# Performance work log

Measured on AMD Instinct MI355X. Metric: run time of the kernel, lower is better.

The kernel has to match this reference:

```python
import jax, jax.numpy as jnp
import numpy as np

N_ATOMS = 2_000_000
D_IN = 128
N_HIDDEN = 16
N_STRUCT = 20_000


def setup_inputs() -> dict:
    key = jax.random.key(0)
    kx, ks, k0, k1, k2 = jax.random.split(key, 5)
    x = jax.random.normal(kx, (N_ATOMS, D_IN), dtype=jnp.float32)
    structure = jnp.sort(jax.random.randint(ks, (N_ATOMS,), 0, N_STRUCT, dtype=jnp.int32))
    # MLP(nin=128, nout=1, nhidden=16, nlayers=2, bias=False, activation=None):
    # Linear(128->16) -> Linear(16->16) -> Linear(16->1), purely linear stack.
    W0 = jax.random.normal(k0, (D_IN, N_HIDDEN), dtype=jnp.float32) / np.sqrt(D_IN)
    W1 = jax.random.normal(k1, (N_HIDDEN, N_HIDDEN), dtype=jnp.float32) / np.sqrt(N_HIDDEN)
    W2 = jax.random.normal(k2, (N_HIDDEN, 1), dtype=jnp.float32) / np.sqrt(N_HIDDEN)
    return {"x": x, "W0": W0, "W1": W1, "W2": W2,
            "structure": structure, "num_structures": N_STRUCT}


def reference(x, W0, W1, W2, structure, num_structures):
    # per-atom tiny MLP: [N, D] -> [N, 1] -> [N]
    h = x @ W0            # [N, 16]
    h = h @ W1            # [N, 16]
    pred = (h @ W2)[:, 0]  # [N]
    # scatter-sum per structure id (torch index_add_ equivalent)
    per_struct = jax.ops.segment_sum(pred, structure, num_segments=num_structures)
    return per_struct[:, None]  # [n_struct, 1]
```

## Files before the change

kernel.cpp:

```cpp
#include <hip/hip_runtime.h>

#define D_IN 128
#define NH   16

__global__ void prep_kernel(const float* __restrict__ W0,
                            const float* __restrict__ W1,
                            const float* __restrict__ W2,
                            float* __restrict__ w,
                            float* __restrict__ out, int m) {
    int i = blockIdx.x * blockDim.x + threadIdx.x;
    if (i < m) out[i] = 0.f;

    if (blockIdx.x == 0) {
        __shared__ float v1[NH];
        int t = threadIdx.x;
        if (t < NH) {
            float s = 0.f;
            #pragma unroll
            for (int k = 0; k < NH; ++k) s += W1[t * NH + k] * W2[k];
            v1[t] = s;
        }
        __syncthreads();
        if (t < D_IN) {
            float s = 0.f;
            #pragma unroll
            for (int j = 0; j < NH; ++j) s += W0[t * NH + j] * v1[j];
            w[t] = s;
        }
    }
}

__global__ __launch_bounds__(256) void predict_scatter_kernel(
        const float* __restrict__ x,
        const int*   __restrict__ sid,
        const float* __restrict__ w,
        float*       __restrict__ out,
        int n, int nTiles) {
    __shared__ float preds[256];

    const int lane  = threadIdx.x & 63;
    const int hlane = threadIdx.x & 31;
    const int hw    = threadIdx.x >> 5;

    const float4 wv = reinterpret_cast<const float4*>(w)[hlane];

    for (int tile = blockIdx.x; tile < nTiles; tile += gridDim.x) {
        const long long tileBase = (long long)tile * 256;

        if (tileBase + 256 <= (long long)n) {
            #pragma unroll 4
            for (int step = 0; step < 32; ++step) {
                const long long atom = tileBase + hw * 32 + step;
                float4 xv = reinterpret_cast<const float4*>(x)[atom * 32 + hlane];
                float d = xv.x * wv.x + xv.y * wv.y + xv.z * wv.z + xv.w * wv.w;
                #pragma unroll
                for (int off = 16; off >= 1; off >>= 1)
                    d += __shfl_xor(d, off, 32);
                if (hlane == 0) preds[hw * 32 + step] = d;
            }
        } else {
            for (int step = 0; step < 32; ++step) {
                const long long atom = tileBase + hw * 32 + step;
                if (atom < (long long)n) {
                    float4 xv = reinterpret_cast<const float4*>(x)[atom * 32 + hlane];
                    float d = xv.x * wv.x + xv.y * wv.y + xv.z * wv.z + xv.w * wv.w;
                    #pragma unroll
                    for (int off = 16; off >= 1; off >>= 1)
                        d += __shfl_xor(d, off, 32);
                    if (hlane == 0) preds[hw * 32 + step] = d;
                }
            }
        }
        __syncthreads();

        {
            const long long g = tileBase + threadIdx.x;
            float p = 0.f;
            int   s = -1;
            if (g < (long long)n) {
                p = preds[threadIdx.x];
                s = sid[g];
            }
            #pragma unroll
            for (int off = 1; off < 64; off <<= 1) {
                float pv = __shfl_up(p, off, 64);
                int   sv = __shfl_up(s, off, 64);
                if (lane >= off && sv == s) p += pv;
            }
            int  sn   = __shfl_down(s, 1, 64);
            bool tail = (lane == 63) || (sn != s);
            if (tail && s >= 0) atomicAdd(&out[s], p);
        }
        __syncthreads();
    }
}

extern "C" void kernel_launch(void* const* d_in, const int* in_sizes, int n_in,
                              void* d_out, int out_size, void* d_ws, size_t ws_size,
                              hipStream_t stream) {
    const float* x   = (const float*)d_in[0];
    const float* W0  = (const float*)d_in[1];
    const float* W1  = (const float*)d_in[2];
    const float* W2  = (const float*)d_in[3];
    const int*   sid = (const int*)d_in[4];
    float*       out = (float*)d_out;
    float*       w   = (float*)d_ws;

    const int n = in_sizes[0] / D_IN;

    {
        int blocks = (out_size + 255) / 256;
        if (blocks < 1) blocks = 1;
        prep_kernel<<<blocks, 256, 0, stream>>>(W0, W1, W2, w, out, out_size);
    }

    {
        const int nTiles  = (n + 255) >> 8;
        int       nblocks = nTiles < 2048 ? nTiles : 2048;
        predict_scatter_kernel<<<nblocks, 256, 0, stream>>>(x, sid, w, out, n, nTiles);
    }
}
```

Before: 184.3 us.

## Process per-wave atom strips with register double-buffering and deferred per-segment reduction

Replaces the tile-based design (half-wave dot products, shared-memory staging, wave-level segmented scan) with one wave per 256-atom strip. Each lane accumulates its share of the dot product across consecutive atoms and only does a full wave reduction plus atomic when the structure id changes. Loads are double-buffered in registers with nontemporal hints, which removes the per-atom shuffles and the block barriers. The cost is a 64-lane reduction at every segment boundary (about every 100 atoms) and a branch that reads sid values per batch.

```diff
diff --git a/kernel.cpp b/kernel.cpp
--- a/kernel.cpp
+++ b/kernel.cpp
@@ -1,7 +1,11 @@
 #include <hip/hip_runtime.h>
+
+typedef float f32x2 __attribute__((ext_vector_type(2)));
 
 #define D_IN 128
 #define NH   16
+#define APW  256
+#define BS   8
 
 __global__ void prep_kernel(const float* __restrict__ W0,
                             const float* __restrict__ W1,
@@ -10,7 +14,6 @@
                             float* __restrict__ out, int m) {
     int i = blockIdx.x * blockDim.x + threadIdx.x;
     if (i < m) out[i] = 0.f;
-
     if (blockIdx.x == 0) {
         __shared__ float v1[NH];
         int t = threadIdx.x;
@@ -30,68 +33,89 @@
     }
 }
 
-__global__ __launch_bounds__(256) void predict_scatter_kernel(
+__device__ __forceinline__ void flush_seg(float r, int seg, float* __restrict__ out) {
+    #pragma unroll
+    for (int off = 32; off >= 1; off >>= 1) r += __shfl_xor(r, off, 64);
+    if ((threadIdx.x & 63) == 0) atomicAdd(out + seg, r);
+}
+
+__global__ __launch_bounds__(256) void main_kernel(
         const float* __restrict__ x,
         const int*   __restrict__ sid,
         const float* __restrict__ w,
         float*       __restrict__ out,
-        int n, int nTiles) {
-    __shared__ float preds[256];
+        int n, int nStrips, int totalWaves) {
+    const int lane   = threadIdx.x & 63;
+    const int waveG  = __builtin_amdgcn_readfirstlane((blockIdx.x << 2) + (threadIdx.x >> 6));
 
-    const int lane  = threadIdx.x & 63;
-    const int hlane = threadIdx.x & 31;
-    const int hw    = threadIdx.x >> 5;
+    const f32x2* __restrict__ x2 = reinterpret_cast<const f32x2*>(x);
+    const f32x2 wv = reinterpret_cast<const f32x2*>(w)[lane];
 
-    const float4 wv = reinterpret_cast<const float4*>(w)[hlane];
+    for (int strip = waveG; strip < nStrips; strip += totalWaves) {
+        const int base  = strip * APW;
+        const int count = min(APW, n - base);
+        const f32x2* __restrict__ xs = x2 + (long long)base * 64 + lane;
 
-    for (int tile = blockIdx.x; tile < nTiles; tile += gridDim.x) {
-        const long long tileBase = (long long)tile * 256;
+        int   cur = sid[base];
+        float r   = 0.f;
 
-        if (tileBase + 256 <= (long long)n) {
-            #pragma unroll 4
-            for (int step = 0; step < 32; ++step) {
-                const long long atom = tileBase + hw * 32 + step;
-                float4 xv = reinterpret_cast<const float4*>(x)[atom * 32 + hlane];
-                float d = xv.x * wv.x + xv.y * wv.y + xv.z * wv.z + xv.w * wv.w;
-                #pragma unroll
-                for (int off = 16; off >= 1; off >>= 1)
-                    d += __shfl_xor(d, off, 32);
-                if (hlane == 0) preds[hw * 32 + step] = d;
+        if (count == APW) {
+            f32x2 A[BS], B[BS];
+            #pragma unroll
+            for (int s = 0; s < BS; ++s) A[s] = __builtin_nontemporal_load(&xs[s * 64]);
+
+            const int NB = APW / BS;
+            for (int ib = 0; ib < NB; ib += 2) {
+                {
+                    const f32x2* p = xs + (ib + 1) * BS * 64;
+                    #pragma unroll
+                    for (int s = 0; s < BS; ++s) B[s] = __builtin_nontemporal_load(&p[s * 64]);
+                }
+                {
+                    const int off = base + ib * BS;
+                    int slast = sid[off + BS - 1];
+                    if (slast == cur) {
+                        #pragma unroll
+                        for (int s = 0; s < BS; ++s) r += A[s].x * wv.x + A[s].y * wv.y;
+                    } else {
+                        #pragma unroll
+                        for (int s = 0; s < BS; ++s) {
+                            int cs = sid[off + s];
+                            if (cs != cur) { flush_seg(r, cur, out); r = 0.f; cur = cs; }
+                            r += A[s].x * wv.x + A[s].y * wv.y;
+                        }
+                    }
+                }
+                if (ib + 2 < NB) {
+                    const f32x2* p = xs + (ib + 2) * BS * 64;
+                    #pragma unroll
+                    for (int s = 0; s < BS; ++s) A[s] = __builtin_nontemporal_load(&p[s * 64]);
+                }
+                {
+                    const int off = base + (ib + 1) * BS;
+                    int slast = sid[off + BS - 1];
+                    if (slast == cur) {
+                        #pragma unroll
+                        for (int s = 0; s < BS; ++s) r += B[s].x * wv.x + B[s].y * wv.y;
+                    } else {
+                        #pragma unroll
+                        for (int s = 0; s < BS; ++s) {
+                            int cs = sid[off + s];
+                            if (cs != cur) { flush_seg(r, cur, out); r = 0.f; cur = cs; }
+                            r += B[s].x * wv.x + B[s].y * wv.y;
+                        }
+                    }
+                }
             }
         } else {
-            for (int step = 0; step < 32; ++step) {
-                const long long atom = tileBase + hw * 32 + step;
-                if (atom < (long long)n) {
-                    float4 xv = reinterpret_cast<const float4*>(x)[atom * 32 + hlane];
-                    float d = xv.x * wv.x + xv.y * wv.y + xv.z * wv.z + xv.w * wv.w;
-                    #pragma unroll
-                    for (int off = 16; off >= 1; off >>= 1)
-                        d += __shfl_xor(d, off, 32);
-                    if (hlane == 0) preds[hw * 32 + step] = d;
-                }
+            for (int s = 0; s < count; ++s) {
+                int cs = sid[base + s];
+                if (cs != cur) { flush_seg(r, cur, out); r = 0.f; cur = cs; }
+                f32x2 xv = xs[s * 64];
+                r += xv.x * wv.x + xv.y * wv.y;
             }
         }
-        __syncthreads();
-
-        {
-            const long long g = tileBase + threadIdx.x;
-            float p = 0.f;
-            int   s = -1;
-            if (g < (long long)n) {
-                p = preds[threadIdx.x];
-                s = sid[g];
-            }
-            #pragma unroll
-            for (int off = 1; off < 64; off <<= 1) {
-                float pv = __shfl_up(p, off, 64);
-                int   sv = __shfl_up(s, off, 64);
-                if (lane >= off && sv == s) p += pv;
-            }
-            int  sn   = __shfl_down(s, 1, 64);
-            bool tail = (lane == 63) || (sn != s);
-            if (tail && s >= 0) atomicAdd(&out[s], p);
-        }
-        __syncthreads();
+        flush_seg(r, cur, out);
     }
 }
 
@@ -115,8 +139,10 @@
     }
 
     {
-        const int nTiles  = (n + 255) >> 8;
-        int       nblocks = nTiles < 2048 ? nTiles : 2048;
-        predict_scatter_kernel<<<nblocks, 256, 0, stream>>>(x, sid, w, out, n, nTiles);
+        const int nStrips = (n + APW - 1) / APW;
+        int nblocks = (nStrips + 3) / 4;
+        if (nblocks > 2048) nblocks = 2048;
+        const int totalWaves = nblocks * 4;
+        main_kernel<<<nblocks, 256, 0, stream>>>(x, sid, w, out, n, nStrips, totalWaves);
     }
 }
```

Measured after the change: 169.8 us. 1.09x faster.
